# Performance work log

Hardware: AMD Instinct MI355X
Metric: run time of the kernel (lower is better)

Reference implementation:

```python
import jax, jax.numpy as jnp
import numpy as np

B, T, H, DK = 4, 2048, 16, 64
F = H * DK
CK, NL = 64, 16  # chunk_size, num left chunks
MIN_VAL = float(np.finfo(np.float16).min)


def chunk_mask(size, ck, nl):
    # row i attends cols [max((i//ck - nl)*ck, 0), (i//ck + 1)*ck)
    i = jnp.arange(size)
    start = jnp.maximum((i // ck - nl) * ck, 0)
    end = (i // ck + 1) * ck
    j = jnp.arange(size)
    return (j[None, :] >= start[:, None]) & (j[None, :] < end[:, None])


def setup_inputs() -> dict:
    rng = jax.random.key(0)
    ks = jax.random.split(rng, 14)
    s = 1.0 / np.sqrt(F)
    mask = jnp.broadcast_to(chunk_mask(T, CK, NL)[None], (B, T, T))  # padding mask all-True & chunk band
    return {
        "query": jax.random.normal(ks[0], (B, T, F), jnp.float32),
        "key": jax.random.normal(ks[1], (B, T, F), jnp.float32),
        "value": jax.random.normal(ks[2], (B, T, F), jnp.float32),
        "pos_emb": jax.random.normal(ks[3], (1, T, F), jnp.float32),
        "mask": mask,
        "Wq": jax.random.normal(ks[4], (F, F), jnp.float32) * s,
        "bq": jnp.zeros((F,), jnp.float32),
        "Wk": jax.random.normal(ks[5], (F, F), jnp.float32) * s,
        "bk": jnp.zeros((F,), jnp.float32),
        "Wv": jax.random.normal(ks[6], (F, F), jnp.float32) * s,
        "bv": jnp.zeros((F,), jnp.float32),
        "Wp": jax.random.normal(ks[7], (F, F), jnp.float32) * s,
        "Wo": jax.random.normal(ks[8], (F, F), jnp.float32) * s,
        "bo": jnp.zeros((F,), jnp.float32),
        "pos_bias_u": jax.random.normal(ks[9], (H, DK), jnp.float32) * 0.05,
        "pos_bias_v": jax.random.normal(ks[10], (H, DK), jnp.float32) * 0.05,
    }


def reference(query, key, value, pos_emb, mask, Wq, bq, Wk, bk, Wv, bv, Wp, Wo, bo, pos_bias_u, pos_bias_v):
    b, t1, _ = query.shape
    t2 = key.shape[1]
    q = (query @ Wq.T + bq).reshape(b, t1, H, DK)            # (b, t1, h, d)
    k = (key @ Wk.T + bk).reshape(b, t2, H, DK).transpose(0, 2, 1, 3)   # (b, h, t2, d)
    v = (value @ Wv.T + bv).reshape(b, t2, H, DK).transpose(0, 2, 1, 3)  # (b, h, t2, d)
    p = (pos_emb @ Wp.T).reshape(pos_emb.shape[0], -1, H, DK).transpose(0, 2, 1, 3)[0]  # (h, t2, d)
    # matrix_ac: content score with bias u; matrix_bd: position score with bias v (no rel_shift in forward)
    matrix_ac = jnp.einsum('bthd,bhsd->bhts', q + pos_bias_u, k)
    matrix_bd = jnp.einsum('bthd,hsd->bhts', q + pos_bias_v, p)
    scores = (matrix_ac + matrix_bd) / np.sqrt(DK)
    m = mask[:, None, :, :]                                   # (b, 1, t1, t2)
    scores = jnp.where(m, scores, MIN_VAL)
    attn = jax.nn.softmax(scores, axis=-1)
    attn = jnp.where(m, attn, 0.0)
    x = jnp.einsum('bhts,bhsd->bthd', attn, v).reshape(b, t1, F)
    return x @ Wo.T + bo
```

## Files before the change

kernel.cpp:

```cpp
#include <hip/hip_runtime.h>
#include <hip/hip_bf16.h>

#define B_ 4
#define T_ 2048
#define H_ 16
#define DK_ 64
#define F_ 1024
#define SCALE_LOG2 0.18033688011112042f

typedef __bf16 bf16x8 __attribute__((ext_vector_type(8)));
typedef __bf16 bf16x4 __attribute__((ext_vector_type(4)));
typedef float f32x4 __attribute__((ext_vector_type(4)));

__device__ __forceinline__ void async_cp16(const void* g, void* l) {
  __builtin_amdgcn_global_load_lds((const __attribute__((address_space(1))) void*)g,
                                   (__attribute__((address_space(3))) void*)l, 16, 0, 0);
}

struct CvtArgs {
  const float* src[9];
  __bf16* dst[9];
  int n[9];
};
__global__ void cvt_all(CvtArgs a) {
  int t = blockIdx.y;
  int i = (blockIdx.x * 256 + threadIdx.x) * 8;
  if (i >= a.n[t]) return;
  const float* in = a.src[t];
  __bf16* out = a.dst[t];
  float4 x = *(const float4*)(in + i);
  float4 y = *(const float4*)(in + i + 4);
  bf16x8 o;
  o[0] = (__bf16)x.x; o[1] = (__bf16)x.y; o[2] = (__bf16)x.z; o[3] = (__bf16)x.w;
  o[4] = (__bf16)y.x; o[5] = (__bf16)y.y; o[6] = (__bf16)y.z; o[7] = (__bf16)y.w;
  *(bf16x8*)(out + i) = o;
}

#define GEMM_MAIN_LOOP(A_, B_ptr, AsP, BsP)                                              \
  for (int k0 = 0; k0 < F_; k0 += 32) {                                                  \
    if (k0) __syncthreads();                                                             \
    for (int ph = 0; ph < 2; ++ph) {                                                     \
      int rb = ph * 64 + wave * 16;                                                      \
      async_cp16(A_ + (m0 + rb + srow) * (long)F_ + k0 + scol, AsP + rb * 32);           \
      async_cp16(B_ptr + (n0 + rb + srow) * (long)F_ + k0 + scol, BsP + rb * 32);        \
    }                                                                                    \
    __syncthreads();                                                                     \
    bf16x8 af[4], bfr[4];                                                                \
    for (int i = 0; i < 4; i++) af[i] = *(const bf16x8*)&AsP[(wr + i * 16 + mrow) * 32 + quad * 8]; \
    for (int j = 0; j < 4; j++) bfr[j] = *(const bf16x8*)&BsP[(wc + j * 16 + mrow) * 32 + quad * 8]; \
    for (int i = 0; i < 4; i++)                                                          \
      for (int j = 0; j < 4; j++)                                                        \
        acc[i][j] = __builtin_amdgcn_mfma_f32_16x16x32_bf16(af[i], bfr[j], acc[i][j], 0, 0, 0); \
  }

__global__ __launch_bounds__(256) void gemm_p(
    const __bf16* __restrict__ Wm, const __bf16* __restrict__ Act,
    __bf16* __restrict__ Ph, const float* __restrict__ vb, float* __restrict__ pbias) {
  __shared__ __bf16 As[128 * 32];
  __shared__ __bf16 Bs[128 * 32];
  const int tid = threadIdx.x;
  const int wave = tid >> 6, lane = tid & 63;
  const int mrow = lane & 15, quad = lane >> 4;
  const long m0 = (long)blockIdx.y * 128;
  const long n0 = (long)blockIdx.x * 128;
  const int wr = (wave >> 1) * 64, wc = (wave & 1) * 64;
  const int srow = lane >> 2, scol = (lane & 3) * 8;
  f32x4 acc[4][4] = {};
  GEMM_MAIN_LOOP(Wm, Act, As, Bs)
  const int h = ((int)m0 + wr) >> 6;
  float s[4] = {0.f, 0.f, 0.f, 0.f};
  for (int i = 0; i < 4; i++) {
    int frow = (int)m0 + wr + i * 16 + quad * 4;
    float4 v4 = *(const float4*)&vb[frow];
    int dbase = frow & 63;
    for (int j = 0; j < 4; j++) {
      int token = (int)n0 + wc + j * 16 + mrow;
      s[j] += v4.x * acc[i][j][0] + v4.y * acc[i][j][1] + v4.z * acc[i][j][2] + v4.w * acc[i][j][3];
      bf16x4 pk;
      pk[0] = (__bf16)acc[i][j][0]; pk[1] = (__bf16)acc[i][j][1];
      pk[2] = (__bf16)acc[i][j][2]; pk[3] = (__bf16)acc[i][j][3];
      *(bf16x4*)&Ph[((long)h * T_ + token) * DK_ + dbase] = pk;
    }
  }
  for (int j = 0; j < 4; j++) {
    float t = s[j];
    t += __shfl_xor(t, 16);
    t += __shfl_xor(t, 32);
    if (quad == 0) {
      int token = (int)n0 + wc + j * 16 + mrow;
      pbias[h * T_ + token] = t;
    }
  }
}

struct GemmQKV {
  const __bf16* W[3];
  const __bf16* Act[3];
  const float* bias[3];
};
__global__ __launch_bounds__(256) void gemm_qkv(
    GemmQKV g, const __bf16* __restrict__ Ph, const float* __restrict__ u,
    const float* __restrict__ pbias, __bf16* __restrict__ Qh, __bf16* __restrict__ Kh,
    __bf16* __restrict__ Vth, float* __restrict__ biasC) {
  __shared__ __align__(16) __bf16 smem[128 * 132];
  __bf16* As = smem;
  __bf16* Bs = smem + 128 * 32;
  const int z = blockIdx.z;
  const __bf16* __restrict__ A = g.W[z];
  const __bf16* __restrict__ Bact = g.Act[z];
  const float* __restrict__ bias = g.bias[z];
  const int tid = threadIdx.x;
  const int wave = tid >> 6, lane = tid & 63;
  const int mrow = lane & 15, quad = lane >> 4;
  const long m0 = (long)blockIdx.y * 128;
  const long n0 = (long)blockIdx.x * 128;
  const int wr = (wave >> 1) * 64, wc = (wave & 1) * 64;
  const int srow = lane >> 2, scol = (lane & 3) * 8;
  f32x4 acc[4][4] = {};
  GEMM_MAIN_LOOP(A, Bact, As, Bs)
  const int h = ((int)m0 + wr) >> 6;
  const int bb = (int)(n0 >> 11);

  if (z == 0) {
    for (int i = 0; i < 4; i++) {
      int frow = (int)m0 + wr + i * 16 + quad * 4;
      float4 b4 = *(const float4*)&bias[frow];
      int dbase = frow & 63;
      for (int j = 0; j < 4; j++) {
        int token = (int)n0 + wc + j * 16 + mrow;
        int tt = token & 2047;
        bf16x4 pk;
        pk[0] = (__bf16)(acc[i][j][0] + b4.x);
        pk[1] = (__bf16)(acc[i][j][1] + b4.y);
        pk[2] = (__bf16)(acc[i][j][2] + b4.z);
        pk[3] = (__bf16)(acc[i][j][3] + b4.w);
        *(bf16x4*)&Qh[(((long)(bb * H_ + h)) * T_ + tt) * DK_ + dbase] = pk;
      }
    }
  } else if (z == 1) {
    float s[4] = {0.f, 0.f, 0.f, 0.f};
    for (int i = 0; i < 4; i++) {
      int frow = (int)m0 + wr + i * 16 + quad * 4;
      float4 b4 = *(const float4*)&bias[frow];
      float4 u4 = *(const float4*)&u[frow];
      int dbase = frow & 63;
      for (int j = 0; j < 4; j++) {
        int token = (int)n0 + wc + j * 16 + mrow;
        int tt = token & 2047;
        float k0v = acc[i][j][0] + b4.x;
        float k1v = acc[i][j][1] + b4.y;
        float k2v = acc[i][j][2] + b4.z;
        float k3v = acc[i][j][3] + b4.w;
        s[j] += u4.x * k0v + u4.y * k1v + u4.z * k2v + u4.w * k3v;
        bf16x4 p4 = *(const bf16x4*)&Ph[((long)h * T_ + tt) * DK_ + dbase];
        bf16x4 pk;
        pk[0] = (__bf16)(k0v + (float)p4[0]);
        pk[1] = (__bf16)(k1v + (float)p4[1]);
        pk[2] = (__bf16)(k2v + (float)p4[2]);
        pk[3] = (__bf16)(k3v + (float)p4[3]);
        *(bf16x4*)&Kh[(((long)(bb * H_ + h)) * T_ + tt) * DK_ + dbase] = pk;
      }
    }
    for (int j = 0; j < 4; j++) {
      float t = s[j];
      t += __shfl_xor(t, 16);
      t += __shfl_xor(t, 32);
      if (quad == 0) {
        int token = (int)n0 + wc + j * 16 + mrow;
        int tt = token & 2047;
        biasC[((long)(bb * H_ + h)) * T_ + tt] = (t + pbias[h * T_ + tt]) * SCALE_LOG2;
      }
    }
  } else {
    __syncthreads();
    for (int i = 0; i < 4; i++) {
      int fl = wr + i * 16 + quad * 4;
      float4 b4 = *(const float4*)&bias[m0 + fl];
      for (int j = 0; j < 4; j++) {
        int tl = wc + j * 16 + mrow;
        bf16x4 pk;
        pk[0] = (__bf16)(acc[i][j][0] + b4.x);
        pk[1] = (__bf16)(acc[i][j][1] + b4.y);
        pk[2] = (__bf16)(acc[i][j][2] + b4.z);
        pk[3] = (__bf16)(acc[i][j][3] + b4.w);
        *(bf16x4*)&smem[tl * 132 + fl] = pk;
      }
    }
    __syncthreads();
    int t0 = (int)(n0 & 2047);
#pragma unroll
    for (int p = 0; p < 8; ++p) {
      int idx = p * 256 + tid;
      int dl = idx >> 4, tch = (idx & 15) * 8;
      bf16x8 o;
#pragma unroll
      for (int k = 0; k < 8; ++k) o[k] = smem[(tch + k) * 132 + dl];
      int hh = ((int)m0 >> 6) + (dl >> 6);
      int d = dl & 63;
      *(bf16x8*)&Vth[(((long)(bb * H_ + hh)) * DK_ + d) * T_ + t0 + tch] = o;
    }
  }
}

__global__ __launch_bounds__(256) void gemm_out(
    const __bf16* __restrict__ A, const __bf16* __restrict__ Bm,
    float* __restrict__ Cout, const float* __restrict__ bias, int N) {
  __shared__ __bf16 As[128 * 32];
  __shared__ __bf16 Bs[128 * 32];
  const int tid = threadIdx.x;
  const int wave = tid >> 6, lane = tid & 63;
  const int mrow = lane & 15, quad = lane >> 4;
  const long m0 = (long)blockIdx.y * 128, n0 = (long)blockIdx.x * 128;
  const int wr = (wave >> 1) * 64, wc = (wave & 1) * 64;
  const int srow = lane >> 2, scol = (lane & 3) * 8;
  f32x4 acc[4][4] = {};
  GEMM_MAIN_LOOP(A, Bm, As, Bs)
  for (int i = 0; i < 4; i++) {
    int row = (int)m0 + wr + i * 16 + quad * 4;
    for (int j = 0; j < 4; j++) {
      int col = (int)n0 + wc + j * 16 + mrow;
      float bval = bias[col];
      for (int r = 0; r < 4; r++)
        Cout[(long)(row + r) * N + col] = acc[i][j][r] + bval;
    }
  }
}

template <int FULL>
__device__ __forceinline__ void attn_step2(
    int s0, long bh, int tid, int wave, int mrow, int quad,
    const __bf16* __restrict__ Kh, const __bf16* __restrict__ Vth,
    const float* __restrict__ Bp, const bf16x8 (&qf)[4][2],
    __bf16* Pl, __bf16* Vt, f32x4 accO[4], f32x4& accL) {
  __syncthreads();
  if (FULL) {
#pragma unroll
    for (int p = 0; p < 4; ++p) {
      int idx = tid + p * 256;
      int row = idx >> 4, colg = (idx & 15) * 8;
      *(bf16x8*)&Vt[row * 136 + colg] =
          *(const bf16x8*)&Vth[(bh * DK_ + row) * T_ + s0 + colg];
    }
  } else {
#pragma unroll
    for (int p = 0; p < 2; ++p) {
      int idx = tid + p * 256;
      int row = idx >> 3, colg = (idx & 7) * 8;
      *(bf16x8*)&Vt[row * 136 + colg] =
          *(const bf16x8*)&Vth[(bh * DK_ + row) * T_ + s0 + colg];
    }
  }
  if (FULL || wave < 2) {
    const int krow = s0 + wave * 32;
    bf16x8 kf[2][2];
#pragma unroll
    for (int nt = 0; nt < 2; ++nt)
#pragma unroll
      for (int kh = 0; kh < 2; ++kh)
        kf[nt][kh] = *(const bf16x8*)&Kh[(bh * T_ + krow + nt * 16 + mrow) * DK_ + kh * 32 + quad * 8];
    float bias01[2] = {Bp[krow + mrow], Bp[krow + 16 + mrow]};
    f32x4 s[4][2];
#pragma unroll
    for (int mt = 0; mt < 4; ++mt)
#pragma unroll
      for (int nt = 0; nt < 2; ++nt) {
        f32x4 a = {0.f, 0.f, 0.f, 0.f};
        a = __builtin_amdgcn_mfma_f32_16x16x32_bf16(qf[mt][0], kf[nt][0], a, 0, 0, 0);
        a = __builtin_amdgcn_mfma_f32_16x16x32_bf16(qf[mt][1], kf[nt][1], a, 0, 0, 0);
        s[mt][nt] = a;
      }
#pragma unroll
    for (int mt = 0; mt < 4; ++mt)
#pragma unroll
      for (int nt = 0; nt < 2; ++nt)
#pragma unroll
        for (int r = 0; r < 4; ++r) {
          float p = __builtin_amdgcn_exp2f(s[mt][nt][r] * SCALE_LOG2 + bias01[nt]);
          Pl[(mt * 16 + quad * 4 + r) * 136 + wave * 32 + nt * 16 + mrow] = (__bf16)p;
        }
  }
  __syncthreads();
  constexpr int NKT = FULL ? 4 : 2;
  bf16x8 ones;
#pragma unroll
  for (int j = 0; j < 8; ++j) ones[j] = (__bf16)1.0f;
  bf16x8 ap[NKT];
#pragma unroll
  for (int kt = 0; kt < NKT; ++kt)
    ap[kt] = *(const bf16x8*)&Pl[(wave * 16 + mrow) * 136 + kt * 32 + quad * 8];
#pragma unroll
  for (int kt = 0; kt < NKT; ++kt) {
    accL = __builtin_amdgcn_mfma_f32_16x16x32_bf16(ap[kt], ones, accL, 0, 0, 0);
#pragma unroll
    for (int nt = 0; nt < 4; ++nt) {
      bf16x8 bv = *(const bf16x8*)&Vt[(nt * 16 + mrow) * 136 + kt * 32 + quad * 8];
      accO[nt] = __builtin_amdgcn_mfma_f32_16x16x32_bf16(ap[kt], bv, accO[nt], 0, 0, 0);
    }
  }
}

__global__ __launch_bounds__(256) void attn_banded(
    const __bf16* __restrict__ Qh, const __bf16* __restrict__ Kh,
    const __bf16* __restrict__ Vth, const float* __restrict__ biasC,
    __bf16* __restrict__ X) {
  __shared__ __bf16 Pl[64 * 136];
  __shared__ __bf16 Vt[64 * 136];
  const int qc = blockIdx.x, h = blockIdx.y, b = blockIdx.z;
  const int tid = threadIdx.x, wave = tid >> 6, lane = tid & 63;
  const int mrow = lane & 15, quad = lane >> 4;
  const long bh = b * H_ + h;
  const int span = (qc >= 16 ? 17 : qc + 1);
  const int s_lo = (qc + 1 - span) * 64, s_hi = (qc + 1) * 64;
  const float* Bp = biasC + bh * T_;
  bf16x8 qf[4][2];
#pragma unroll
  for (int mt = 0; mt < 4; ++mt)
#pragma unroll
    for (int kh = 0; kh < 2; ++kh)
      qf[mt][kh] = *(const bf16x8*)&Qh[(bh * T_ + qc * 64 + mt * 16 + mrow) * DK_ + kh * 32 + quad * 8];
  f32x4 accO[4] = {};
  f32x4 accL = {0.f, 0.f, 0.f, 0.f};
  int s0 = s_lo;
  if (span & 1) {
    attn_step2<0>(s0, bh, tid, wave, mrow, quad, Kh, Vth, Bp, qf, Pl, Vt, accO, accL);
    s0 += 64;
  }
  for (; s0 < s_hi; s0 += 128)
    attn_step2<1>(s0, bh, tid, wave, mrow, quad, Kh, Vth, Bp, qf, Pl, Vt, accO, accL);
#pragma unroll
  for (int r = 0; r < 4; ++r) {
    float inv = 1.0f / accL[r];
    int t = qc * 64 + wave * 16 + quad * 4 + r;
#pragma unroll
    for (int nt = 0; nt < 4; ++nt)
      X[((long)(b * T_ + t) * H_ + h) * DK_ + nt * 16 + mrow] = (__bf16)(accO[nt][r] * inv);
  }
}

extern "C" void kernel_launch(void* const* d_in, const int* in_sizes, int n_in,
                              void* d_out, int out_size, void* d_ws, size_t ws_size,
                              hipStream_t stream) {
  (void)in_sizes; (void)n_in; (void)out_size; (void)ws_size;
  const float* query = (const float*)d_in[0];
  const float* key   = (const float*)d_in[1];
  const float* value = (const float*)d_in[2];
  const float* pos   = (const float*)d_in[3];
  const float* Wq = (const float*)d_in[5];
  const float* bq = (const float*)d_in[6];
  const float* Wk = (const float*)d_in[7];
  const float* bk = (const float*)d_in[8];
  const float* Wv = (const float*)d_in[9];
  const float* bv = (const float*)d_in[10];
  const float* Wp = (const float*)d_in[11];
  const float* Wo = (const float*)d_in[12];
  const float* bo = (const float*)d_in[13];
  const float* pu = (const float*)d_in[14];
  const float* pvb = (const float*)d_in[15];

  const long NQ = (long)B_ * T_ * F_;
  const long NP = (long)T_ * F_;
  const long NW = (long)F_ * F_;
  char* ws = (char*)d_ws;
  __bf16* qb  = (__bf16*)ws; ws += NQ * 2;
  __bf16* kb  = (__bf16*)ws; ws += NQ * 2;
  __bf16* vbm = (__bf16*)ws; ws += NQ * 2;
  __bf16* pb  = (__bf16*)ws; ws += NP * 2;
  __bf16* wqb = (__bf16*)ws; ws += NW * 2;
  __bf16* wkb = (__bf16*)ws; ws += NW * 2;
  __bf16* wvb = (__bf16*)ws; ws += NW * 2;
  __bf16* wpb = (__bf16*)ws; ws += NW * 2;
  __bf16* wob = (__bf16*)ws; ws += NW * 2;
  __bf16* Qh  = (__bf16*)ws; ws += NQ * 2;
  __bf16* Kh  = (__bf16*)ws; ws += NQ * 2;
  __bf16* Vth = (__bf16*)ws; ws += NQ * 2;
  __bf16* Ph  = (__bf16*)ws; ws += NP * 2;
  float*  biasC = (float*)ws; ws += (long)B_ * H_ * T_ * 4;
  float*  pbias = (float*)ws; ws += (long)H_ * T_ * 4;
  __bf16* Xb  = qb;

  {
    CvtArgs ca;
    ca.src[0] = query; ca.dst[0] = qb;  ca.n[0] = (int)NQ;
    ca.src[1] = key;   ca.dst[1] = kb;  ca.n[1] = (int)NQ;
    ca.src[2] = value; ca.dst[2] = vbm; ca.n[2] = (int)NQ;
    ca.src[3] = pos;   ca.dst[3] = pb;  ca.n[3] = (int)NP;
    ca.src[4] = Wq;    ca.dst[4] = wqb; ca.n[4] = (int)NW;
    ca.src[5] = Wk;    ca.dst[5] = wkb; ca.n[5] = (int)NW;
    ca.src[6] = Wv;    ca.dst[6] = wvb; ca.n[6] = (int)NW;
    ca.src[7] = Wp;    ca.dst[7] = wpb; ca.n[7] = (int)NW;
    ca.src[8] = Wo;    ca.dst[8] = wob; ca.n[8] = (int)NW;
    cvt_all<<<dim3(4096, 9), 256, 0, stream>>>(ca);
  }
  gemm_p<<<dim3(16, 8), 256, 0, stream>>>(wpb, pb, Ph, pvb, pbias);
  {
    GemmQKV g;
    g.W[0] = wqb; g.Act[0] = qb;  g.bias[0] = bq;
    g.W[1] = wkb; g.Act[1] = kb;  g.bias[1] = bk;
    g.W[2] = wvb; g.Act[2] = vbm; g.bias[2] = bv;
    gemm_qkv<<<dim3(64, 8, 3), 256, 0, stream>>>(g, Ph, pu, pbias, Qh, Kh, Vth, biasC);
  }
  attn_banded<<<dim3(32, 16, 4), 256, 0, stream>>>(Qh, Kh, Vth, biasC, Xb);
  gemm_out<<<dim3(8, 64), 256, 0, stream>>>(Xb, wob, (float*)d_out, bo, F_);
}
```

Before: 423.9 us.

## Rewrite banded attention as per-wave transposed MFMA flow without block barriers

Each wave now owns 16 query rows and walks the key band in 32-key steps on its own. It computes S^T with transposed MFMA operands and loads V fragments directly from global memory. It passes P through a small per-wave LDS scratch instead of block-wide shared tiles with __syncthreads, and sums the softmax denominator with lane shuffles instead of an MFMA against a vector of ones. The launch becomes a flat 1D grid that maps blocks of the same (b,h) pair onto the same XCD for L2 locality. This trades shared-memory reuse of K and V across the four waves for no block barriers and fewer ops, at the cost of redundant global/L2 loads.

```diff
diff --git a/kernel.cpp b/kernel.cpp
--- a/kernel.cpp
+++ b/kernel.cpp
@@ -226,114 +226,73 @@
   }
 }
 
-template <int FULL>
-__device__ __forceinline__ void attn_step2(
-    int s0, long bh, int tid, int wave, int mrow, int quad,
-    const __bf16* __restrict__ Kh, const __bf16* __restrict__ Vth,
-    const float* __restrict__ Bp, const bf16x8 (&qf)[4][2],
-    __bf16* Pl, __bf16* Vt, f32x4 accO[4], f32x4& accL) {
-  __syncthreads();
-  if (FULL) {
-#pragma unroll
-    for (int p = 0; p < 4; ++p) {
-      int idx = tid + p * 256;
-      int row = idx >> 4, colg = (idx & 15) * 8;
-      *(bf16x8*)&Vt[row * 136 + colg] =
-          *(const bf16x8*)&Vth[(bh * DK_ + row) * T_ + s0 + colg];
-    }
-  } else {
-#pragma unroll
-    for (int p = 0; p < 2; ++p) {
-      int idx = tid + p * 256;
-      int row = idx >> 3, colg = (idx & 7) * 8;
-      *(bf16x8*)&Vt[row * 136 + colg] =
-          *(const bf16x8*)&Vth[(bh * DK_ + row) * T_ + s0 + colg];
-    }
-  }
-  if (FULL || wave < 2) {
-    const int krow = s0 + wave * 32;
-    bf16x8 kf[2][2];
-#pragma unroll
-    for (int nt = 0; nt < 2; ++nt)
-#pragma unroll
-      for (int kh = 0; kh < 2; ++kh)
-        kf[nt][kh] = *(const bf16x8*)&Kh[(bh * T_ + krow + nt * 16 + mrow) * DK_ + kh * 32 + quad * 8];
-    float bias01[2] = {Bp[krow + mrow], Bp[krow + 16 + mrow]};
-    f32x4 s[4][2];
-#pragma unroll
-    for (int mt = 0; mt < 4; ++mt)
-#pragma unroll
-      for (int nt = 0; nt < 2; ++nt) {
-        f32x4 a = {0.f, 0.f, 0.f, 0.f};
-        a = __builtin_amdgcn_mfma_f32_16x16x32_bf16(qf[mt][0], kf[nt][0], a, 0, 0, 0);
-        a = __builtin_amdgcn_mfma_f32_16x16x32_bf16(qf[mt][1], kf[nt][1], a, 0, 0, 0);
-        s[mt][nt] = a;
-      }
-#pragma unroll
-    for (int mt = 0; mt < 4; ++mt)
-#pragma unroll
-      for (int nt = 0; nt < 2; ++nt)
-#pragma unroll
-        for (int r = 0; r < 4; ++r) {
-          float p = __builtin_amdgcn_exp2f(s[mt][nt][r] * SCALE_LOG2 + bias01[nt]);
-          Pl[(mt * 16 + quad * 4 + r) * 136 + wave * 32 + nt * 16 + mrow] = (__bf16)p;
-        }
-  }
-  __syncthreads();
-  constexpr int NKT = FULL ? 4 : 2;
-  bf16x8 ones;
-#pragma unroll
-  for (int j = 0; j < 8; ++j) ones[j] = (__bf16)1.0f;
-  bf16x8 ap[NKT];
-#pragma unroll
-  for (int kt = 0; kt < NKT; ++kt)
-    ap[kt] = *(const bf16x8*)&Pl[(wave * 16 + mrow) * 136 + kt * 32 + quad * 8];
-#pragma unroll
-  for (int kt = 0; kt < NKT; ++kt) {
-    accL = __builtin_amdgcn_mfma_f32_16x16x32_bf16(ap[kt], ones, accL, 0, 0, 0);
-#pragma unroll
-    for (int nt = 0; nt < 4; ++nt) {
-      bf16x8 bv = *(const bf16x8*)&Vt[(nt * 16 + mrow) * 136 + kt * 32 + quad * 8];
-      accO[nt] = __builtin_amdgcn_mfma_f32_16x16x32_bf16(ap[kt], bv, accO[nt], 0, 0, 0);
-    }
-  }
-}
-
 __global__ __launch_bounds__(256) void attn_banded(
     const __bf16* __restrict__ Qh, const __bf16* __restrict__ Kh,
     const __bf16* __restrict__ Vth, const float* __restrict__ biasC,
     __bf16* __restrict__ X) {
-  __shared__ __bf16 Pl[64 * 136];
-  __shared__ __bf16 Vt[64 * 136];
-  const int qc = blockIdx.x, h = blockIdx.y, b = blockIdx.z;
+  __shared__ __bf16 Pw[4][16 * 34];
+  const int bid = blockIdx.x;
+  const int xcd = bid & 7, loc = bid >> 3;
+  const int grp = loc >> 5, qc = loc & 31;
+  const int pr = xcd * 8 + grp;
+  const int b = pr >> 4, h = pr & 15;
   const int tid = threadIdx.x, wave = tid >> 6, lane = tid & 63;
   const int mrow = lane & 15, quad = lane >> 4;
   const long bh = b * H_ + h;
   const int span = (qc >= 16 ? 17 : qc + 1);
-  const int s_lo = (qc + 1 - span) * 64, s_hi = (qc + 1) * 64;
-  const float* Bp = biasC + bh * T_;
-  bf16x8 qf[4][2];
-#pragma unroll
-  for (int mt = 0; mt < 4; ++mt)
-#pragma unroll
-    for (int kh = 0; kh < 2; ++kh)
-      qf[mt][kh] = *(const bf16x8*)&Qh[(bh * T_ + qc * 64 + mt * 16 + mrow) * DK_ + kh * 32 + quad * 8];
+  const int s_lo = (qc + 1 - span) * 64;
+  const float* __restrict__ Bp = biasC + bh * T_;
+  __bf16* Pl = &Pw[wave][0];
+  const int qrow = qc * 64 + wave * 16 + mrow;
+  bf16x8 qf0 = *(const bf16x8*)&Qh[(bh * T_ + qrow) * DK_ + quad * 8];
+  bf16x8 qf1 = *(const bf16x8*)&Qh[(bh * T_ + qrow) * DK_ + 32 + quad * 8];
   f32x4 accO[4] = {};
-  f32x4 accL = {0.f, 0.f, 0.f, 0.f};
-  int s0 = s_lo;
-  if (span & 1) {
-    attn_step2<0>(s0, bh, tid, wave, mrow, quad, Kh, Vth, Bp, qf, Pl, Vt, accO, accL);
-    s0 += 64;
-  }
-  for (; s0 < s_hi; s0 += 128)
-    attn_step2<1>(s0, bh, tid, wave, mrow, quad, Kh, Vth, Bp, qf, Pl, Vt, accO, accL);
-#pragma unroll
-  for (int r = 0; r < 4; ++r) {
-    float inv = 1.0f / accL[r];
-    int t = qc * 64 + wave * 16 + quad * 4 + r;
-#pragma unroll
-    for (int nt = 0; nt < 4; ++nt)
-      X[((long)(b * T_ + t) * H_ + h) * DK_ + nt * 16 + mrow] = (__bf16)(accO[nt][r] * inv);
+  float lsum = 0.f;
+  const int nsteps = span * 2;
+  for (int g = 0; g < nsteps; ++g) {
+    const int ks = s_lo + g * 32;
+    bf16x8 kf[2][2];
+#pragma unroll
+    for (int nt = 0; nt < 2; ++nt)
+#pragma unroll
+      for (int kh = 0; kh < 2; ++kh)
+        kf[nt][kh] = *(const bf16x8*)&Kh[(bh * T_ + ks + nt * 16 + mrow) * DK_ + kh * 32 + quad * 8];
+    bf16x8 vf[4];
+#pragma unroll
+    for (int dt = 0; dt < 4; ++dt)
+      vf[dt] = *(const bf16x8*)&Vth[(bh * DK_ + dt * 16 + mrow) * T_ + ks + quad * 8];
+#pragma unroll
+    for (int nt = 0; nt < 2; ++nt) {
+      f32x4 s = {0.f, 0.f, 0.f, 0.f};
+      s = __builtin_amdgcn_mfma_f32_16x16x32_bf16(kf[nt][0], qf0, s, 0, 0, 0);
+      s = __builtin_amdgcn_mfma_f32_16x16x32_bf16(kf[nt][1], qf1, s, 0, 0, 0);
+      float4 b4 = *(const float4*)&Bp[ks + nt * 16 + quad * 4];
+      float p0 = __builtin_amdgcn_exp2f(s[0] * SCALE_LOG2 + b4.x);
+      float p1 = __builtin_amdgcn_exp2f(s[1] * SCALE_LOG2 + b4.y);
+      float p2 = __builtin_amdgcn_exp2f(s[2] * SCALE_LOG2 + b4.z);
+      float p3 = __builtin_amdgcn_exp2f(s[3] * SCALE_LOG2 + b4.w);
+      lsum += (p0 + p1) + (p2 + p3);
+      bf16x4 pk;
+      pk[0] = (__bf16)p0; pk[1] = (__bf16)p1; pk[2] = (__bf16)p2; pk[3] = (__bf16)p3;
+      *(bf16x4*)&Pl[mrow * 34 + nt * 16 + quad * 4] = pk;
+    }
+    bf16x8 pf = *(const bf16x8*)&Pl[mrow * 34 + quad * 8];
+#pragma unroll
+    for (int dt = 0; dt < 4; ++dt)
+      accO[dt] = __builtin_amdgcn_mfma_f32_16x16x32_bf16(vf[dt], pf, accO[dt], 0, 0, 0);
+  }
+  lsum += __shfl_xor(lsum, 16);
+  lsum += __shfl_xor(lsum, 32);
+  const float inv = 1.0f / lsum;
+  const int t = qc * 64 + wave * 16 + mrow;
+#pragma unroll
+  for (int dt = 0; dt < 4; ++dt) {
+    bf16x4 o;
+    o[0] = (__bf16)(accO[dt][0] * inv);
+    o[1] = (__bf16)(accO[dt][1] * inv);
+    o[2] = (__bf16)(accO[dt][2] * inv);
+    o[3] = (__bf16)(accO[dt][3] * inv);
+    *(bf16x4*)&X[((long)(b * T_ + t) * H_ + h) * DK_ + dt * 16 + quad * 4] = o;
   }
 }
 
@@ -399,6 +358,6 @@
     g.W[2] = wvb; g.Act[2] = vbm; g.bias[2] = bv;
     gemm_qkv<<<dim3(64, 8, 3), 256, 0, stream>>>(g, Ph, pu, pbias, Qh, Kh, Vth, biasC);
   }
-  attn_banded<<<dim3(32, 16, 4), 256, 0, stream>>>(Qh, Kh, Vth, biasC, Xb);
+  attn_banded<<<dim3(2048), 256, 0, stream>>>(Qh, Kh, Vth, biasC, Xb);
   gemm_out<<<dim3(8, 64), 256, 0, stream>>>(Xb, wob, (float*)d_out, bo, F_);
 }
```

Measured after the change: 558.3 us. +31.7%, slower.
